# Optimization experiments

Measured on AMD Instinct MI355X. Metric: run time of the kernel, lower is better.

The kernel has to match this reference:

```python
import jax, jax.numpy as jnp
import numpy as np

INDIM = 1024
OUTDIM = 2048
BATCH = 8192


def _kaiming_uniform(key, shape):
    # torch kaiming_uniform_ default: a=sqrt(5) -> gain=sqrt(2/(1+5))=sqrt(1/3),
    # fan_in = shape[0] (first dim for 2D), bound = gain*sqrt(3/fan_in) = 1/sqrt(fan_in)
    fan_in = shape[0]
    bound = 1.0 / np.sqrt(fan_in)
    return jax.random.uniform(key, shape, dtype=jnp.float32, minval=-bound, maxval=bound)


def setup_inputs() -> dict:
    key = jax.random.key(0)
    kx, kp = jax.random.split(key)
    x = jax.random.normal(kx, (BATCH, INDIM), dtype=jnp.float32)
    prototypes = _kaiming_uniform(kp, (INDIM, OUTDIM))
    return {"x": x, "prototypes": prototypes}


def reference(x, prototypes):
    # score[b, o] = -sum_i (x[b,i] - P[i,o])^2
    #             = -(||x_b||^2 - 2 x_b . P_:,o + ||P_:,o||^2)
    x_sq = jnp.sum(x * x, axis=1, keepdims=True)          # [B, 1]
    p_sq = jnp.sum(prototypes * prototypes, axis=0)       # [O]
    cross = jnp.matmul(x, prototypes)                      # [B, O] GEMM
    return 2.0 * cross - x_sq - p_sq[None, :]
```

## Files before the change

kernel.cpp:

```cpp
#include <hip/hip_runtime.h>
#include <hip/hip_bf16.h>
#include <cstdint>

#define BATCH  8192
#define INDIM  1024
#define OUTDIM 2048

typedef float  f32x4   __attribute__((ext_vector_type(4)));
typedef float  f32x16  __attribute__((ext_vector_type(16)));
typedef __bf16 bf16x8  __attribute__((ext_vector_type(8)));
typedef unsigned short u16x4 __attribute__((ext_vector_type(4)));
typedef unsigned short u16x8 __attribute__((ext_vector_type(8)));

__device__ __forceinline__ uint16_t f2b(float f) {
    __hip_bfloat16 h = __float2bfloat16(f);
    return __builtin_bit_cast(uint16_t, h);
}

__device__ __forceinline__ void async_copy16(const void* g, void* l) {
    __builtin_amdgcn_global_load_lds(
        (__attribute__((address_space(1))) void*)(g),
        (__attribute__((address_space(3))) void*)(l),
        16, 0, 0);
}

__device__ __forceinline__ int swkey(int r) { return (r ^ (r >> 3)) & 7; }

__global__ __launch_bounds__(256) void prep_x(const float* __restrict__ x,
                                              uint16_t* __restrict__ xbf,
                                              float* __restrict__ xsq) {
    const int wave = threadIdx.x >> 6;
    const int lane = threadIdx.x & 63;
    const int row  = blockIdx.x * 4 + wave;
    const f32x4* src = (const f32x4*)(x + (size_t)row * INDIM);
    u16x4* dst = (u16x4*)(xbf + (size_t)row * INDIM);
    float s = 0.f;
#pragma unroll
    for (int w = 0; w < 4; ++w) {
        const f32x4 v = src[lane + w * 64];
        s += v.x * v.x + v.y * v.y + v.z * v.z + v.w * v.w;
        u16x4 o;
        o.x = f2b(v.x); o.y = f2b(v.y); o.z = f2b(v.z); o.w = f2b(v.w);
        dst[lane + w * 64] = o;
    }
#pragma unroll
    for (int off = 32; off > 0; off >>= 1) s += __shfl_down(s, off);
    if (lane == 0) xsq[row] = s;
}

__global__ __launch_bounds__(256) void prep_p(const float* __restrict__ P,
                                              uint16_t* __restrict__ ptbf,
                                              float* __restrict__ psq_part) {
    __shared__ float tile[64][33];
    __shared__ float psums[32];
    const int tid = threadIdx.x;
    const int o0  = blockIdx.x * 32;
    const int k0  = blockIdx.y * 256;
    const int kk  = tid >> 3;
    const int oq  = tid & 7;
    const int so  = tid >> 3;
    const int skc = (tid & 7) * 8;
    float a4[4] = {0.f, 0.f, 0.f, 0.f};
    if (tid < 32) psums[tid] = 0.f;
    for (int st = 0; st < 4; ++st) {
        __syncthreads();
#pragma unroll
        for (int r2 = 0; r2 < 2; ++r2) {
            const int k = r2 * 32 + kk;
            const float4 v = *(const float4*)(P + (size_t)(k0 + st * 64 + k) * OUTDIM + o0 + oq * 4);
            tile[k][oq * 4 + 0] = v.x;
            tile[k][oq * 4 + 1] = v.y;
            tile[k][oq * 4 + 2] = v.z;
            tile[k][oq * 4 + 3] = v.w;
            a4[0] += v.x * v.x; a4[1] += v.y * v.y;
            a4[2] += v.z * v.z; a4[3] += v.w * v.w;
        }
        __syncthreads();
        u16x8 w;
#pragma unroll
        for (int j = 0; j < 8; ++j) w[j] = f2b(tile[skc + j][so]);
        *(u16x8*)(ptbf + (size_t)(o0 + so) * INDIM + k0 + st * 64 + skc) = w;
    }
#pragma unroll
    for (int e = 0; e < 4; ++e) atomicAdd(&psums[oq * 4 + e], a4[e]);
    __syncthreads();
    if (tid < 32) psq_part[(size_t)blockIdx.y * OUTDIM + o0 + tid] = psums[tid];
}

#define TM 128
#define TN 128
#define BK 64

__global__ __launch_bounds__(256) void gemm_ep(const uint16_t* __restrict__ xbf,
                                               const uint16_t* __restrict__ ptbf,
                                               const float* __restrict__ xsq,
                                               const float* __restrict__ psq_part,
                                               float* __restrict__ out) {
    __shared__ __align__(16) uint16_t As[TM * BK];
    __shared__ __align__(16) uint16_t Bs[TN * BK];

    const int tid  = threadIdx.x;
    const int m0   = blockIdx.x * TM;
    const int n0   = blockIdx.y * TN;
    const int wave = tid >> 6;
    const int lane = tid & 63;
    const int wm   = (wave >> 1) * 64;
    const int wn   = (wave & 1) * 64;
    const int l31  = lane & 31;
    const int half = lane >> 5;

    f32x16 acc[2][2];
#pragma unroll
    for (int i = 0; i < 2; ++i)
#pragma unroll
        for (int j = 0; j < 2; ++j)
#pragma unroll
            for (int e = 0; e < 16; ++e) acc[i][j][e] = 0.f;

    for (int kb = 0; kb < INDIM; kb += BK) {
#pragma unroll
        for (int t = 0; t < 4; ++t) {
            const int id = t * 256 + tid;
            const int r  = id >> 3;
            const int cs = id & 7;
            const int cg = cs ^ swkey(r);
            async_copy16(xbf  + (size_t)(m0 + r) * INDIM + kb + cg * 8, As + id * 8);
            async_copy16(ptbf + (size_t)(n0 + r) * INDIM + kb + cg * 8, Bs + id * 8);
        }
        __syncthreads();

#pragma unroll
        for (int ks = 0; ks < 4; ++ks) {
            const int c = ks * 2 + half;
            bf16x8 a[2], b[2];
#pragma unroll
            for (int i = 0; i < 2; ++i) {
                const int r = wm + i * 32 + l31;
                a[i] = *(const bf16x8*)(As + r * BK + (c ^ swkey(r)) * 8);
            }
#pragma unroll
            for (int j = 0; j < 2; ++j) {
                const int r = wn + j * 32 + l31;
                b[j] = *(const bf16x8*)(Bs + r * BK + (c ^ swkey(r)) * 8);
            }
#pragma unroll
            for (int i = 0; i < 2; ++i)
#pragma unroll
                for (int j = 0; j < 2; ++j)
                    acc[i][j] = __builtin_amdgcn_mfma_f32_32x32x16_bf16(a[i], b[j], acc[i][j], 0, 0, 0);
        }
        __syncthreads();
    }

    const float* xsq_w = xsq + m0 + wm;
    float ps[2];
#pragma unroll
    for (int j = 0; j < 2; ++j) {
        const int n = n0 + wn + j * 32 + l31;
        ps[j] = psq_part[n] + psq_part[OUTDIM + n] +
                psq_part[2 * OUTDIM + n] + psq_part[3 * OUTDIM + n];
    }
#pragma unroll
    for (int i = 0; i < 2; ++i) {
#pragma unroll
        for (int rg = 0; rg < 16; ++rg) {
            const int rloc = (rg & 3) + 8 * (rg >> 2) + 4 * half;
            const float xs = xsq_w[i * 32 + rloc];
            float* orow = out + (size_t)(m0 + wm + i * 32 + rloc) * OUTDIM + n0 + wn + l31;
#pragma unroll
            for (int j = 0; j < 2; ++j)
                orow[j * 32] = 2.f * acc[i][j][rg] - xs - ps[j];
        }
    }
}

__global__ void fallback_kernel(const float* __restrict__ x,
                                const float* __restrict__ P,
                                float* __restrict__ out) {
    const int o = blockIdx.x * blockDim.x + threadIdx.x;
    const int b = blockIdx.y;
    float cr = 0.f, xq = 0.f, pq = 0.f;
    for (int i = 0; i < INDIM; ++i) {
        const float xv = x[(size_t)b * INDIM + i];
        const float pv = P[(size_t)i * OUTDIM + o];
        cr += xv * pv; xq += xv * xv; pq += pv * pv;
    }
    out[(size_t)b * OUTDIM + o] = 2.f * cr - xq - pq;
}

extern "C" void kernel_launch(void* const* d_in, const int* in_sizes, int n_in,
                              void* d_out, int out_size, void* d_ws, size_t ws_size,
                              hipStream_t stream) {
    (void)in_sizes; (void)n_in; (void)out_size;
    const float* x = (const float*)d_in[0];
    const float* P = (const float*)d_in[1];
    float* out = (float*)d_out;

    const size_t xbf_bytes = (size_t)BATCH * INDIM * 2;
    const size_t pt_bytes  = (size_t)OUTDIM * INDIM * 2;
    const size_t xsq_bytes = (size_t)BATCH * 4;
    const size_t psq_bytes = (size_t)4 * OUTDIM * 4;
    const size_t need = xbf_bytes + pt_bytes + xsq_bytes + psq_bytes;

    if (ws_size < need) {
        fallback_kernel<<<dim3(OUTDIM / 256, BATCH), 256, 0, stream>>>(x, P, out);
        return;
    }

    uint16_t* xbf      = (uint16_t*)d_ws;
    uint16_t* ptbf     = (uint16_t*)((char*)d_ws + xbf_bytes);
    float*    xsq      = (float*)((char*)d_ws + xbf_bytes + pt_bytes);
    float*    psq_part = xsq + BATCH;

    prep_x<<<BATCH / 4, 256, 0, stream>>>(x, xbf, xsq);
    prep_p<<<dim3(OUTDIM / 32, INDIM / 256), 256, 0, stream>>>(P, ptbf, psq_part);
    gemm_ep<<<dim3(BATCH / TM, OUTDIM / TN), 256, 0, stream>>>(xbf, ptbf, xsq, psq_part, out);
}
```

Before: 136.1 us.

## Switch cross-term GEMM from bf16 to fp8 MFMA with scaled prototypes

```diff
diff --git a/kernel.cpp b/kernel.cpp
--- a/kernel.cpp
+++ b/kernel.cpp
@@ -8,13 +8,13 @@
 
 typedef float  f32x4   __attribute__((ext_vector_type(4)));
 typedef float  f32x16  __attribute__((ext_vector_type(16)));
-typedef __bf16 bf16x8  __attribute__((ext_vector_type(8)));
-typedef unsigned short u16x4 __attribute__((ext_vector_type(4)));
-typedef unsigned short u16x8 __attribute__((ext_vector_type(8)));
-
-__device__ __forceinline__ uint16_t f2b(float f) {
-    __hip_bfloat16 h = __float2bfloat16(f);
-    return __builtin_bit_cast(uint16_t, h);
+typedef int    i32x2   __attribute__((ext_vector_type(2)));
+
+__device__ __forceinline__ uint32_t pk_fp8x4(float a, float b, float c, float d) {
+    uint32_t v = 0;
+    v = __builtin_amdgcn_cvt_pk_fp8_f32(a, b, v, false);
+    v = __builtin_amdgcn_cvt_pk_fp8_f32(c, d, v, true);
+    return v;
 }
 
 __device__ __forceinline__ void async_copy16(const void* g, void* l) {
@@ -24,24 +24,22 @@
         16, 0, 0);
 }
 
-__device__ __forceinline__ int swkey(int r) { return (r ^ (r >> 3)) & 7; }
+__device__ __forceinline__ int k4(int r) { return (r ^ (r >> 2)) & 3; }
 
 __global__ __launch_bounds__(256) void prep_x(const float* __restrict__ x,
-                                              uint16_t* __restrict__ xbf,
+                                              uint8_t* __restrict__ xq8,
                                               float* __restrict__ xsq) {
     const int wave = threadIdx.x >> 6;
     const int lane = threadIdx.x & 63;
     const int row  = blockIdx.x * 4 + wave;
     const f32x4* src = (const f32x4*)(x + (size_t)row * INDIM);
-    u16x4* dst = (u16x4*)(xbf + (size_t)row * INDIM);
+    uint32_t* dst = (uint32_t*)(xq8 + (size_t)row * INDIM);
     float s = 0.f;
 #pragma unroll
     for (int w = 0; w < 4; ++w) {
         const f32x4 v = src[lane + w * 64];
         s += v.x * v.x + v.y * v.y + v.z * v.z + v.w * v.w;
-        u16x4 o;
-        o.x = f2b(v.x); o.y = f2b(v.y); o.z = f2b(v.z); o.w = f2b(v.w);
-        dst[lane + w * 64] = o;
+        dst[lane + w * 64] = pk_fp8x4(v.x, v.y, v.z, v.w);
     }
 #pragma unroll
     for (int off = 32; off > 0; off >>= 1) s += __shfl_down(s, off);
@@ -49,7 +47,7 @@
 }
 
 __global__ __launch_bounds__(256) void prep_p(const float* __restrict__ P,
-                                              uint16_t* __restrict__ ptbf,
+                                              uint8_t* __restrict__ pt8,
                                               float* __restrict__ psq_part) {
     __shared__ float tile[64][33];
     __shared__ float psums[32];
@@ -76,10 +74,12 @@
             a4[2] += v.z * v.z; a4[3] += v.w * v.w;
         }
         __syncthreads();
-        u16x8 w;
-#pragma unroll
-        for (int j = 0; j < 8; ++j) w[j] = f2b(tile[skc + j][so]);
-        *(u16x8*)(ptbf + (size_t)(o0 + so) * INDIM + k0 + st * 64 + skc) = w;
+        i32x2 w;
+        w.x = pk_fp8x4(tile[skc + 0][so] * 32.f, tile[skc + 1][so] * 32.f,
+                       tile[skc + 2][so] * 32.f, tile[skc + 3][so] * 32.f);
+        w.y = pk_fp8x4(tile[skc + 4][so] * 32.f, tile[skc + 5][so] * 32.f,
+                       tile[skc + 6][so] * 32.f, tile[skc + 7][so] * 32.f);
+        *(i32x2*)(pt8 + (size_t)(o0 + so) * INDIM + k0 + st * 64 + skc) = w;
     }
 #pragma unroll
     for (int e = 0; e < 4; ++e) atomicAdd(&psums[oq * 4 + e], a4[e]);
@@ -89,15 +89,15 @@
 
 #define TM 128
 #define TN 128
-#define BK 64
-
-__global__ __launch_bounds__(256) void gemm_ep(const uint16_t* __restrict__ xbf,
-                                               const uint16_t* __restrict__ ptbf,
+#define BKB 64
+
+__global__ __launch_bounds__(256) void gemm_ep(const uint8_t* __restrict__ xq8,
+                                               const uint8_t* __restrict__ pt8,
                                                const float* __restrict__ xsq,
                                                const float* __restrict__ psq_part,
                                                float* __restrict__ out) {
-    __shared__ __align__(16) uint16_t As[TM * BK];
-    __shared__ __align__(16) uint16_t Bs[TN * BK];
+    __shared__ __align__(16) uint8_t As[TM * BKB];
+    __shared__ __align__(16) uint8_t Bs[TN * BKB];
 
     const int tid  = threadIdx.x;
     const int m0   = blockIdx.x * TM;
@@ -117,37 +117,36 @@
 #pragma unroll
             for (int e = 0; e < 16; ++e) acc[i][j][e] = 0.f;
 
-    for (int kb = 0; kb < INDIM; kb += BK) {
-#pragma unroll
-        for (int t = 0; t < 4; ++t) {
+    for (int kb = 0; kb < INDIM; kb += BKB) {
+#pragma unroll
+        for (int t = 0; t < 2; ++t) {
             const int id = t * 256 + tid;
-            const int r  = id >> 3;
-            const int cs = id & 7;
-            const int cg = cs ^ swkey(r);
-            async_copy16(xbf  + (size_t)(m0 + r) * INDIM + kb + cg * 8, As + id * 8);
-            async_copy16(ptbf + (size_t)(n0 + r) * INDIM + kb + cg * 8, Bs + id * 8);
+            const int r  = id >> 2;
+            const int q  = id & 3;
+            const int qg = q ^ k4(r);
+            async_copy16(xq8 + (size_t)(m0 + r) * INDIM + kb + qg * 16, As + id * 16);
+            async_copy16(pt8 + (size_t)(n0 + r) * INDIM + kb + qg * 16, Bs + id * 16);
         }
         __syncthreads();
 
 #pragma unroll
         for (int ks = 0; ks < 4; ++ks) {
-            const int c = ks * 2 + half;
-            bf16x8 a[2], b[2];
+            long a[2], b[2];
 #pragma unroll
             for (int i = 0; i < 2; ++i) {
                 const int r = wm + i * 32 + l31;
-                a[i] = *(const bf16x8*)(As + r * BK + (c ^ swkey(r)) * 8);
+                a[i] = *(const long*)(As + r * BKB + (ks ^ k4(r)) * 16 + half * 8);
             }
 #pragma unroll
             for (int j = 0; j < 2; ++j) {
                 const int r = wn + j * 32 + l31;
-                b[j] = *(const bf16x8*)(Bs + r * BK + (c ^ swkey(r)) * 8);
+                b[j] = *(const long*)(Bs + r * BKB + (ks ^ k4(r)) * 16 + half * 8);
             }
 #pragma unroll
             for (int i = 0; i < 2; ++i)
 #pragma unroll
                 for (int j = 0; j < 2; ++j)
-                    acc[i][j] = __builtin_amdgcn_mfma_f32_32x32x16_bf16(a[i], b[j], acc[i][j], 0, 0, 0);
+                    acc[i][j] = __builtin_amdgcn_mfma_f32_32x32x16_fp8_fp8(a[i], b[j], acc[i][j], 0, 0, 0);
         }
         __syncthreads();
     }
@@ -169,7 +168,7 @@
             float* orow = out + (size_t)(m0 + wm + i * 32 + rloc) * OUTDIM + n0 + wn + l31;
 #pragma unroll
             for (int j = 0; j < 2; ++j)
-                orow[j * 32] = 2.f * acc[i][j][rg] - xs - ps[j];
+                orow[j * 32] = 0.0625f * acc[i][j][rg] - xs - ps[j];
         }
     }
 }
@@ -196,23 +195,23 @@
     const float* P = (const float*)d_in[1];
     float* out = (float*)d_out;
 
-    const size_t xbf_bytes = (size_t)BATCH * INDIM * 2;
-    const size_t pt_bytes  = (size_t)OUTDIM * INDIM * 2;
+    const size_t xq_bytes  = (size_t)BATCH * INDIM;
+    const size_t pt_bytes  = (size_t)OUTDIM * INDIM;
     const size_t xsq_bytes = (size_t)BATCH * 4;
     const size_t psq_bytes = (size_t)4 * OUTDIM * 4;
-    const size_t need = xbf_bytes + pt_bytes + xsq_bytes + psq_bytes;
+    const size_t need = xq_bytes + pt_bytes + xsq_bytes + psq_bytes;
 
     if (ws_size < need) {
         fallback_kernel<<<dim3(OUTDIM / 256, BATCH), 256, 0, stream>>>(x, P, out);
         return;
     }
 
-    uint16_t* xbf      = (uint16_t*)d_ws;
-    uint16_t* ptbf     = (uint16_t*)((char*)d_ws + xbf_bytes);
-    float*    xsq      = (float*)((char*)d_ws + xbf_bytes + pt_bytes);
-    float*    psq_part = xsq + BATCH;
-
-    prep_x<<<BATCH / 4, 256, 0, stream>>>(x, xbf, xsq);
-    prep_p<<<dim3(OUTDIM / 32, INDIM / 256), 256, 0, stream>>>(P, ptbf, psq_part);
-    gemm_ep<<<dim3(BATCH / TM, OUTDIM / TN), 256, 0, stream>>>(xbf, ptbf, xsq, psq_part, out);
-}
+    uint8_t* xq8      = (uint8_t*)d_ws;
+    uint8_t* pt8      = (uint8_t*)d_ws + xq_bytes;
+    float*   xsq      = (float*)((char*)d_ws + xq_bytes + pt_bytes);
+    float*   psq_part = xsq + BATCH;
+
+    prep_x<<<BATCH / 4, 256, 0, stream>>>(x, xq8, xsq);
+    prep_p<<<dim3(OUTDIM / 32, INDIM / 256), 256, 0, stream>>>(P, pt8, psq_part);
+    gemm_ep<<<dim3(BATCH / TM, OUTDIM / TN), 256, 0, stream>>>(xq8, pt8, xsq, psq_part, out);
+}
```

After: 125.0 us. -8.2%, faster.
